# Kernel tuning notes

Measured on AMD Instinct MI355X. Metric: run time of the kernel, lower is better.

Reference implementation:

```python
import jax, jax.numpy as jnp
import numpy as np

T_STEPS, B, NMUL = 365, 20000, 4
NEARZERO = 1e-06

_BOUNDS = {
    'parBETA': (1.0, 6.0), 'parFC': (50.0, 1000.0), 'parK0': (0.05, 0.9),
    'parK1': (0.01, 0.5), 'parK2': (0.001, 0.2), 'parLP': (0.2, 1.0),
    'parPERC': (0.0, 10.0), 'parUZL': (0.0, 100.0), 'parTT': (-2.5, 2.5),
    'parCFMAX': (0.5, 10.0), 'parCFR': (0.0, 0.1), 'parCWH': (0.0, 0.2),
    'parBETAET': (0.3, 5.0), 'parC': (0.0, 1.0),
}


def setup_inputs() -> dict:
    key = jax.random.key(0)
    kf, kt, kp, *pkeys = jax.random.split(key, 3 + len(_BOUNDS))
    # forcing (T, B, 3): [prcp (mm/d), tmean (degC), pet (mm/d)]
    prcp = jax.random.uniform(kf, (T_STEPS, B), jnp.float32) * 10.0
    tmean = jax.random.normal(kt, (T_STEPS, B), jnp.float32) * 10.0
    pet = jax.random.uniform(kp, (T_STEPS, B), jnp.float32) * 5.0
    inp = {'forcing': jnp.stack([prcp, tmean, pet], axis=-1)}
    for k_rng, (name, (lo, hi)) in zip(pkeys, _BOUNDS.items()):
        inp[name] = jax.random.uniform(k_rng, (B, NMUL), jnp.float32, lo, hi)
    return inp


def _hbv_scan(forcing, parTT, parCFMAX, parCFR, parCWH, parFC, parBETA, parLP,
              parBETAET, parC, parPERC, parK0, parK1, parK2, parUZL):
    eps = NEARZERO
    nmul = parTT.shape[-1]
    n_grid = forcing.shape[1]
    # expand forcing to (T, B, nmul)
    Pm = jnp.broadcast_to(forcing[:, :, 0:1], forcing.shape[:2] + (nmul,))
    Tm = jnp.broadcast_to(forcing[:, :, 1:2], forcing.shape[:2] + (nmul,))
    PETm = jnp.broadcast_to(forcing[:, :, 2:3], forcing.shape[:2] + (nmul,))

    snow0 = jnp.full((n_grid, nmul), eps, forcing.dtype)
    zeros = jnp.zeros((n_grid, nmul), forcing.dtype)

    def step(carry, x):
        snow, melt, sm, suz, slz = carry
        p, t_val, pet = x
        temp_diff = t_val - parTT
        is_rain = temp_diff > 0.0
        rain = jnp.where(is_rain, p, 0.0)
        snow_input = jnp.where(is_rain, 0.0, p)
        snow1 = snow + snow_input
        pot_melt = parCFMAX * jnp.maximum(temp_diff, 0.0)
        melt_amount = jnp.minimum(pot_melt, snow1)
        snow2 = snow1 - melt_amount
        melt1 = melt + melt_amount
        pot_refreeze = parCFR * parCFMAX * jnp.maximum(-temp_diff, 0.0)
        refreeze = jnp.minimum(pot_refreeze, melt1)
        snow_out = snow2 + refreeze
        melt2 = melt1 - refreeze
        tosoil = jnp.maximum(melt2 - parCWH * snow_out, 0.0)
        melt_out = melt2 - tosoil
        soil_wet = jnp.clip(jnp.power(jnp.maximum(sm / parFC, eps), parBETA), 0.0, 1.0)
        recharge = (rain + tosoil) * soil_wet
        sm1 = sm + rain + tosoil - recharge
        excess = jnp.maximum(sm1 - parFC, 0.0)
        sm2 = sm1 - excess
        ef1 = jnp.clip(sm2 / (parLP * parFC), 0.0, 1.0)
        evapfactor = jnp.clip(jnp.power(jnp.maximum(ef1, eps), parBETAET), 0.0, 1.0)
        etact = jnp.minimum(pet * evapfactor, sm2)
        sm_ae = jnp.maximum(sm2 - etact, eps)
        sm_ratio = jnp.minimum(sm_ae / parFC, 1.0)
        capillary = jnp.minimum(slz, parC * slz * (1.0 - sm_ratio))
        sm_out = jnp.maximum(sm_ae + capillary, eps)
        slz_ac = jnp.maximum(slz - capillary, eps)
        suz1 = suz + recharge + excess
        perc_flux = jnp.minimum(suz1, parPERC)
        suz2 = suz1 - perc_flux
        slz1 = slz_ac + perc_flux
        q0 = parK0 * jnp.maximum(suz2 - parUZL, 0.0)
        suz3 = suz2 - q0
        q1 = parK1 * suz3
        suz_out = suz3 - q1
        q2 = parK2 * slz1
        slz_out = slz1 - q2
        q = q0 + q1 + q2
        return (snow_out, melt_out, sm_out, suz_out, slz_out), q

    _, Qsim = jax.lax.scan(step, (snow0, zeros, zeros, zeros, zeros), (Pm, Tm, PETm))
    return Qsim  # (T, B, nmul)


def reference(forcing, parTT, parCFMAX, parCFR, parCWH, parFC, parBETA, parLP,
              parBETAET, parC, parPERC, parK0, parK1, parK2, parUZL):
    Qsim = _hbv_scan(forcing, parTT, parCFMAX, parCFR, parCWH, parFC, parBETA,
                     parLP, parBETAET, parC, parPERC, parK0, parK1, parK2, parUZL)
    Qsim_avg = Qsim.mean(axis=-1)  # 'streamflow' (T, B)
    return (Qsim_avg, Qsim)
```

## Files before the change

kernel.cpp:

```cpp
#include <hip/hip_runtime.h>

#define TSTEPS 365
#define BGRID  20000
#define NMUL   4
#define NEARZERO 1e-6f
#define PF 4
#define V  2

struct F3 { float p, t, pet; };

__device__ __forceinline__ float pair_swap(float x) {
    int a = __builtin_amdgcn_update_dpp(0, __float_as_int(x),
                                        0xB1 , 0xF, 0xF, true);
    return __int_as_float(a);
}

__device__ __forceinline__ float fast_log2(float x) { return __builtin_amdgcn_logf(x); }
__device__ __forceinline__ float fast_exp2(float x) { return __builtin_amdgcn_exp2f(x); }

__global__ __launch_bounds__(64) __attribute__((amdgpu_waves_per_eu(1, 2)))
void hbv_fwd(
    const float* __restrict__ forcing,
    const float* __restrict__ pBETA,  const float* __restrict__ pFC,
    const float* __restrict__ pK0,    const float* __restrict__ pK1,
    const float* __restrict__ pK2,    const float* __restrict__ pLP,
    const float* __restrict__ pPERC,  const float* __restrict__ pUZL,
    const float* __restrict__ pTT,    const float* __restrict__ pCFMAX,
    const float* __restrict__ pCFR,   const float* __restrict__ pCWH,
    const float* __restrict__ pBETAET,const float* __restrict__ pC,
    float* __restrict__ out_avg,
    float* __restrict__ out_q)
{
    const int tid = blockIdx.x * 64 + threadIdx.x;
    const int b  = tid >> 1;
    const int c0 = (b << 2) + (tid & 1);

    float parBETA[V], parFC[V], parK0[V], parK1[V], parK2[V], parPERC[V],
          parUZL[V], parTT[V], parCFMAX[V], parCWH[V], parBETAET[V], parC[V],
          refreeze_coef[V], inv_FC[V], inv_LPFC[V];
#pragma unroll
    for (int v = 0; v < V; ++v) {
        const int c = c0 + 2 * v;
        parBETA[v]   = pBETA[c];   parFC[v]   = pFC[c];
        parK0[v]     = pK0[c];     parK1[v]   = pK1[c];
        parK2[v]     = pK2[c];     parPERC[v] = pPERC[c];
        parUZL[v]    = pUZL[c];    parTT[v]   = pTT[c];
        parCFMAX[v]  = pCFMAX[c];  parCWH[v]  = pCWH[c];
        parBETAET[v] = pBETAET[c]; parC[v]    = pC[c];
        refreeze_coef[v] = pCFR[c] * parCFMAX[v];
        inv_FC[v]   = 1.0f / parFC[v];
        inv_LPFC[v] = 1.0f / (pLP[c] * parFC[v]);
    }

    float snow[V], melt[V], sm[V], suz[V], slz[V];
#pragma unroll
    for (int v = 0; v < V; ++v) {
        snow[v] = NEARZERO; melt[v] = 0.0f; sm[v] = 0.0f; suz[v] = 0.0f; slz[v] = 0.0f;
    }

    const F3* __restrict__ fp = (const F3*)forcing + b;
    float* __restrict__ qq = out_q + c0;
    float* __restrict__ qa = out_avg + b;

    F3 buf[PF];
#pragma unroll
    for (int i = 0; i < PF; ++i) { buf[i] = *fp; fp += BGRID; }

    auto step = [&](const F3 fv) {
        float q[V];
#pragma unroll
        for (int v = 0; v < V; ++v) {
            const float temp_diff = fv.t - parTT[v];
            const bool  is_rain = temp_diff > 0.0f;
            const float rain       = is_rain ? fv.p : 0.0f;
            const float snow_input = is_rain ? 0.0f : fv.p;
            float snow1 = snow[v] + snow_input;
            const float pot_melt = parCFMAX[v] * fmaxf(temp_diff, 0.0f);
            const float melt_amount = fminf(pot_melt, snow1);
            snow1 -= melt_amount;
            float melt1 = melt[v] + melt_amount;
            const float pot_refreeze = refreeze_coef[v] * fmaxf(-temp_diff, 0.0f);
            const float refreeze = fminf(pot_refreeze, melt1);
            snow[v] = snow1 + refreeze;
            melt1 -= refreeze;
            const float tosoil = fmaxf(melt1 - parCWH[v] * snow[v], 0.0f);
            melt[v] = melt1 - tosoil;

            const float x1 = fmaxf(sm[v] * inv_FC[v], NEARZERO);
            const float soil_wet = fminf(fast_exp2(parBETA[v] * fast_log2(x1)), 1.0f);
            const float rt = rain + tosoil;
            const float recharge = rt * soil_wet;
            float sm1 = sm[v] + rt - recharge;
            const float excess = fmaxf(sm1 - parFC[v], 0.0f);
            sm1 -= excess;
            const float ef1 = fminf(sm1 * inv_LPFC[v], 1.0f);
            const float x2 = fmaxf(ef1, NEARZERO);
            const float evapfactor = fminf(fast_exp2(parBETAET[v] * fast_log2(x2)), 1.0f);
            const float etact = fminf(fv.pet * evapfactor, sm1);
            const float sm_ae = fmaxf(sm1 - etact, NEARZERO);
            const float sm_ratio = fminf(sm_ae * inv_FC[v], 1.0f);
            const float capillary = fminf(slz[v], parC[v] * slz[v] * (1.0f - sm_ratio));
            sm[v] = fmaxf(sm_ae + capillary, NEARZERO);
            float slz1 = fmaxf(slz[v] - capillary, NEARZERO);

            float suz1 = suz[v] + recharge + excess;
            const float perc_flux = fminf(suz1, parPERC[v]);
            suz1 -= perc_flux;
            slz1 += perc_flux;
            const float q0 = parK0[v] * fmaxf(suz1 - parUZL[v], 0.0f);
            suz1 -= q0;
            const float q1 = parK1[v] * suz1;
            suz[v] = suz1 - q1;
            const float q2 = parK2[v] * slz1;
            slz[v] = slz1 - q2;
            q[v] = q0 + q1 + q2;
        }

        qq[0] = q[0];
        qq[2] = q[1];
        qq += BGRID * NMUL;
        const float h  = q[0] + q[1];
        const float qs = h + pair_swap(h);
        *qa = qs * 0.25f;
        qa += BGRID;
    };

    constexpr int MAINC = ((TSTEPS - PF) / PF) * PF;
#pragma clang loop unroll(disable)
    for (int base = 0; base < MAINC; base += PF) {
#pragma unroll
        for (int j = 0; j < PF; ++j) {
            const F3 fv = buf[j];
            buf[j] = *fp; fp += BGRID;
            step(fv);
        }
    }
#pragma unroll
    for (int j = 0; j < PF; ++j) {
        const F3 fv = buf[j];
        if (j < TSTEPS - MAINC - PF) { buf[j] = *fp; fp += BGRID; }
        step(fv);
    }
#pragma unroll
    for (int j = 0; j < TSTEPS - MAINC - PF; ++j) {
        step(buf[j]);
    }
}

extern "C" void kernel_launch(void* const* d_in, const int* in_sizes, int n_in,
                              void* d_out, int out_size, void* d_ws, size_t ws_size,
                              hipStream_t stream) {
    const float* forcing = (const float*)d_in[0];

    float* out_avg = (float*)d_out;
    float* out_q   = out_avg + (size_t)TSTEPS * BGRID;

    const int total = BGRID * NMUL / V;
    const int block = 64;
    const int grid  = total / block;
    hbv_fwd<<<grid, block, 0, stream>>>(forcing,
        (const float*)d_in[1], (const float*)d_in[2], (const float*)d_in[3],
        (const float*)d_in[4], (const float*)d_in[5], (const float*)d_in[6],
        (const float*)d_in[7], (const float*)d_in[8], (const float*)d_in[9],
        (const float*)d_in[10], (const float*)d_in[11], (const float*)d_in[12],
        (const float*)d_in[13], (const float*)d_in[14],
        out_avg, out_q);
}
```

Before: 295.2 us.

## Double-buffer forcing loads and defer output stores across chunks of 8 steps

The time loop is restructured into 8-step chunks with two forcing buffers and two output buffers. The loads for the next chunk are issued before the current chunk is computed, and the stores of the previous chunk's results are deferred and interleaved with computation. This replaces the per-step rolling prefetch of depth 4. The aim is to hide global memory latency in a kernel that runs very few waves. The cost is higher register use, from 2×8 F3 buffers plus 2×8×2 result values.

```diff
diff --git a/kernel.cpp b/kernel.cpp
--- a/kernel.cpp
+++ b/kernel.cpp
@@ -4,8 +4,10 @@
 #define BGRID  20000
 #define NMUL   4
 #define NEARZERO 1e-6f
-#define PF 4
-#define V  2
+#define C    8
+#define V    2
+#define NCH  (TSTEPS / C)
+#define TAIL (TSTEPS - NCH * C)
 
 struct F3 { float p, t, pet; };
 
@@ -17,6 +19,22 @@
 
 __device__ __forceinline__ float fast_log2(float x) { return __builtin_amdgcn_logf(x); }
 __device__ __forceinline__ float fast_exp2(float x) { return __builtin_amdgcn_exp2f(x); }
+
+#define LOAD_CHUNK(BUF, N)                                                  \
+    _Pragma("unroll")                                                       \
+    for (int j_ = 0; j_ < (N); ++j_) { BUF[j_] = *fp; fp += BGRID; }
+
+#define STORE_CHUNK(QS, N)                                                  \
+    _Pragma("unroll")                                                       \
+    for (int j_ = 0; j_ < (N); ++j_) {                                      \
+        qq[0] = QS[j_][0]; qq[2] = QS[j_][1]; qq += BGRID * NMUL;           \
+        const float h_ = QS[j_][0] + QS[j_][1];                             \
+        *qa = (h_ + pair_swap(h_)) * 0.25f; qa += BGRID;                    \
+    }
+
+#define COMPUTE_CHUNK(BUF, QO, N)                                           \
+    _Pragma("unroll")                                                       \
+    for (int j_ = 0; j_ < (N); ++j_) { step(BUF[j_], QO[j_]); }
 
 __global__ __launch_bounds__(64) __attribute__((amdgpu_waves_per_eu(1, 2)))
 void hbv_fwd(
@@ -62,12 +80,7 @@
     float* __restrict__ qq = out_q + c0;
     float* __restrict__ qa = out_avg + b;
 
-    F3 buf[PF];
-#pragma unroll
-    for (int i = 0; i < PF; ++i) { buf[i] = *fp; fp += BGRID; }
-
-    auto step = [&](const F3 fv) {
-        float q[V];
+    auto step = [&](const F3 fv, float (&qo)[V]) {
 #pragma unroll
         for (int v = 0; v < V; ++v) {
             const float temp_diff = fv.t - parTT[v];
@@ -113,38 +126,36 @@
             suz[v] = suz1 - q1;
             const float q2 = parK2[v] * slz1;
             slz[v] = slz1 - q2;
-            q[v] = q0 + q1 + q2;
+            qo[v] = q0 + q1 + q2;
         }
-
-        qq[0] = q[0];
-        qq[2] = q[1];
-        qq += BGRID * NMUL;
-        const float h  = q[0] + q[1];
-        const float qs = h + pair_swap(h);
-        *qa = qs * 0.25f;
-        qa += BGRID;
     };
 
-    constexpr int MAINC = ((TSTEPS - PF) / PF) * PF;
+    F3 fA[C], fB[C];
+    float qA[C][V], qB[C][V];
+
+    LOAD_CHUNK(fA, C);
+
+    LOAD_CHUNK(fB, C);
+    COMPUTE_CHUNK(fA, qA, C);
+
 #pragma clang loop unroll(disable)
-    for (int base = 0; base < MAINC; base += PF) {
-#pragma unroll
-        for (int j = 0; j < PF; ++j) {
-            const F3 fv = buf[j];
-            buf[j] = *fp; fp += BGRID;
-            step(fv);
-        }
+    for (int p = 0; p < 21; ++p) {
+        LOAD_CHUNK(fA, C);
+        STORE_CHUNK(qA, C);
+        COMPUTE_CHUNK(fB, qB, C);
+        LOAD_CHUNK(fB, C);
+        STORE_CHUNK(qB, C);
+        COMPUTE_CHUNK(fA, qA, C);
     }
-#pragma unroll
-    for (int j = 0; j < PF; ++j) {
-        const F3 fv = buf[j];
-        if (j < TSTEPS - MAINC - PF) { buf[j] = *fp; fp += BGRID; }
-        step(fv);
-    }
-#pragma unroll
-    for (int j = 0; j < TSTEPS - MAINC - PF; ++j) {
-        step(buf[j]);
-    }
+    LOAD_CHUNK(fA, C);
+    STORE_CHUNK(qA, C);
+    COMPUTE_CHUNK(fB, qB, C);
+    LOAD_CHUNK(fB, TAIL);
+    STORE_CHUNK(qB, C);
+    COMPUTE_CHUNK(fA, qA, C);
+    STORE_CHUNK(qA, C);
+    COMPUTE_CHUNK(fB, qB, TAIL);
+    STORE_CHUNK(qB, TAIL);
 }
 
 extern "C" void kernel_launch(void* const* d_in, const int* in_sizes, int n_in,
```

After: 286.2 us. 1.03x faster.
